# Kernel tuning notes

Measured on AMD Instinct MI355X. Metric: run time of the kernel, lower is better.

## Reference

```python
import jax, jax.numpy as jnp
import numpy as np

B, C, H, W = 8, 192, 64, 64
RED = 8
CR = C // RED  # 24


def prelu(x, a):
    # a is a single shared slope (PyTorch nn.PReLU() default num_parameters=1)
    return jnp.where(x >= 0, x, a * x)


def conv1x1(x, w, b):
    # x: [B,C,H,W], w: [O,C], b: [O] -> [B,O,H,W]
    return jnp.einsum('bchw,oc->bohw', x, w) + b[None, :, None, None]


def setup_inputs() -> dict:
    key = jax.random.key(0)
    ks = jax.random.split(key, 7)
    scale1 = 1.0 / np.sqrt(C)
    return {
        'x': jax.random.normal(ks[0], (B, C, H, W), dtype=jnp.float32),
        'w1': jax.random.uniform(ks[1], (CR, C), jnp.float32, -scale1, scale1),
        'b1': jnp.zeros((CR,), jnp.float32),
        'a1': jnp.full((1,), 0.25, jnp.float32),
        'w2': jax.random.uniform(ks[2], (CR, C), jnp.float32, -scale1, scale1),
        'b2': jnp.zeros((CR,), jnp.float32),
        'a2': jnp.full((1,), 0.25, jnp.float32),
        'wa': jax.random.uniform(ks[3], (C, C), jnp.float32, -scale1, scale1),
        'ba': jnp.zeros((C,), jnp.float32),
        'aa': jnp.full((1,), 0.25, jnp.float32),
    }


def reference(x, w1, b1, a1, w2, b2, a2, wa, ba, aa):
    b, c, h, w = x.shape
    hw = h * w
    q = prelu(conv1x1(x, w1, b1), a1)          # [B,Cr,H,W]
    k = prelu(conv1x1(x, w2, b2), a2)          # [B,Cr,H,W]
    v = prelu(conv1x1(x, wa, ba), aa)          # [B,C,H,W]
    q = q.reshape(b, -1, hw).transpose(0, 2, 1)   # [B,HW,Cr]
    k = k.reshape(b, -1, hw)                      # [B,Cr,HW]
    score = jax.nn.softmax(jnp.einsum('bnc,bcm->bnm', q, k), axis=2)  # [B,HW,HW]
    v = v.reshape(b, c, hw).transpose(0, 2, 1)    # [B,HW,C]
    out = jnp.einsum('bnm,bmc->bnc', score, v)    # [B,HW,C]
    return out.transpose(0, 2, 1).reshape(b, c, h, w)
```

## Files before the change

### kernel.cpp

```cpp
#include <hip/hip_runtime.h>
#include <hip/hip_fp16.h>

#define HW 4096
#define NC 192
#define NB 8
#define DQK 32
#define LOG2E 1.4426950408889634f
#define THR 8.0f

typedef _Float16 f16x8 __attribute__((ext_vector_type(8)));
typedef float f32x4 __attribute__((ext_vector_type(4)));
typedef unsigned int u32x4 __attribute__((ext_vector_type(4)));

static __device__ __forceinline__ unsigned int pkrtz(float a, float b) {
  auto h = __builtin_amdgcn_cvt_pkrtz(a, b);
  return __builtin_bit_cast(unsigned int, h);
}
static __device__ __forceinline__ unsigned short f2h_bits(float f) {
  _Float16 h = (_Float16)f;
  union { _Float16 h; unsigned short u; } cv; cv.h = h; return cv.u;
}

__global__ void wtrans_kernel(
    const float* __restrict__ w1, const float* __restrict__ b1, const float* __restrict__ a1,
    const float* __restrict__ w2, const float* __restrict__ b2, const float* __restrict__ a2,
    const float* __restrict__ wa, const float* __restrict__ ba, const float* __restrict__ aa,
    float* __restrict__ wt)
{
  const int c = blockIdx.x;
  const int o = threadIdx.x;
  if (o >= 240) return;
  float v;
  if (c < 192) {
    if (o < 24)      v = w1[o * 192 + c];
    else if (o < 48) v = w2[(o - 24) * 192 + c];
    else             v = wa[(o - 48) * 192 + c];
  } else if (c == 192) {
    v = (o < 24) ? b1[o] : (o < 48) ? b2[o - 24] : ba[o - 48];
  } else {
    v = (o < 24) ? a1[0] : (o < 48) ? a2[0] : aa[0];
  }
  wt[c * 240 + o] = v;
}

__global__ __launch_bounds__(256) void proj_kernel(
    const float* __restrict__ x, const float* __restrict__ wt,
    unsigned short* __restrict__ Qn, unsigned short* __restrict__ Kn,
    unsigned short* __restrict__ Vt)
{
  const int g   = blockIdx.y;
  const int tid = threadIdx.x;
  const int bp  = (blockIdx.x * 256 + tid) * 2;
  const int b   = bp >> 12;
  const int pos = bp & (HW - 1);

  const float* xb = x + (size_t)b * NC * HW + pos;
  float acc0[16], acc1[16];
  #pragma unroll
  for (int o = 0; o < 16; ++o) { acc0[o] = 0.f; acc1[o] = 0.f; }

  #pragma unroll 4
  for (int c = 0; c < 192; ++c) {
    float2 xv = *reinterpret_cast<const float2*>(xb + (size_t)c * HW);
    const float* wr = wt + c * 240 + g * 16;
    #pragma unroll
    for (int o = 0; o < 16; ++o) {
      float w = wr[o];
      acc0[o] = fmaf(w, xv.x, acc0[o]);
      acc1[o] = fmaf(w, xv.y, acc1[o]);
    }
  }

  const float* brow = wt + 192 * 240 + g * 16;
  const float* srow = wt + 193 * 240 + g * 16;
  unsigned short h0[16], h1[16];
  #pragma unroll
  for (int o = 0; o < 16; ++o) {
    float bias = brow[o], sm1 = srow[o] - 1.f;
    float v0 = acc0[o] + bias; v0 += fminf(v0, 0.f) * sm1;
    float v1 = acc1[o] + bias; v1 += fminf(v1, 0.f) * sm1;
    h0[o] = f2h_bits(v0);
    h1[o] = f2h_bits(v1);
  }

  if (g >= 3) {
    const int vch0 = g * 16 - 48;
    unsigned int* vp = reinterpret_cast<unsigned int*>(
        Vt + ((size_t)b * NC + vch0) * HW + pos);
    #pragma unroll
    for (int o = 0; o < 16; ++o)
      vp[o * (HW / 2)] = (unsigned int)h0[o] | ((unsigned int)h1[o] << 16);
  } else {
    u32x4 lo0, hi0, lo1, hi1;
    #pragma unroll
    for (int j = 0; j < 4; ++j) {
      lo0[j] = (unsigned int)h0[2 * j] | ((unsigned int)h0[2 * j + 1] << 16);
      hi0[j] = (unsigned int)h0[8 + 2 * j] | ((unsigned int)h0[9 + 2 * j] << 16);
      lo1[j] = (unsigned int)h1[2 * j] | ((unsigned int)h1[2 * j + 1] << 16);
      hi1[j] = (unsigned int)h1[8 + 2 * j] | ((unsigned int)h1[9 + 2 * j] << 16);
    }
    const size_t bpos = (size_t)b * HW + pos;
    if (g == 0) {
      u32x4* q0 = reinterpret_cast<u32x4*>(Qn + bpos * DQK);
      q0[0] = lo0; q0[1] = hi0;
      u32x4* q1 = reinterpret_cast<u32x4*>(Qn + (bpos + 1) * DQK);
      q1[0] = lo1; q1[1] = hi1;
    } else if (g == 1) {
      *reinterpret_cast<u32x4*>(Qn + bpos * DQK + 16) = lo0;
      *reinterpret_cast<u32x4*>(Kn + bpos * DQK) = hi0;
      *reinterpret_cast<u32x4*>(Qn + (bpos + 1) * DQK + 16) = lo1;
      *reinterpret_cast<u32x4*>(Kn + (bpos + 1) * DQK) = hi1;
    } else {
      u32x4* k0 = reinterpret_cast<u32x4*>(Kn + bpos * DQK + 8);
      k0[0] = lo0; k0[1] = hi0;
      u32x4* k1 = reinterpret_cast<u32x4*>(Kn + (bpos + 1) * DQK + 8);
      k1[0] = lo1; k1[1] = hi1;
    }
  }
}

__global__ __launch_bounds__(512, 4) void flash_kernel(
    const unsigned short* __restrict__ Qn, const unsigned short* __restrict__ Kn,
    const unsigned short* __restrict__ Vt, float* __restrict__ out)
{
  const int b    = blockIdx.y;
  const int q0   = blockIdx.x * 64;
  const int tid  = threadIdx.x;
  const int w    = tid >> 6;
  const int half = w >> 2;
  const int wi   = w & 3;
  const int lane = tid & 63;
  const int lq   = lane & 15;
  const int lk   = lane >> 4;

  __shared__ u32x4 Pex[2][4][2][64];
  __shared__ float alphaL[2][4][16];
  __shared__ float mlL[2][2][64];
  __shared__ f32x4 Obuf[4][64][13];

  const int mbase = half * (HW / 2);
  const int sigb  = 8 * (lq >> 2) + (lq & 3);

  f16x8 qfrag = *reinterpret_cast<const f16x8*>(
      Qn + ((size_t)b * HW + q0 + 16 * wi + lq) * DQK + 8 * lk);

  float m = -1e30f, l = 0.f;
  f32x4 O[12];
  #pragma unroll
  for (int i = 0; i < 12; ++i) O[i] = (f32x4){0.f, 0.f, 0.f, 0.f};

  const unsigned short* Kb = Kn + (size_t)b * HW * DQK;
  const unsigned short* Vb = Vt + (size_t)b * NC * HW;

  for (int it = 0; it < HW / 2 / 64; ++it) {
    const int m0 = mbase + it * 64;
    f32x4 s[4];
    #pragma unroll
    for (int t = 0; t < 4; ++t) {
      const int mo = m0 + sigb + 32 * (t & 1) + 4 * (t >> 1);
      f16x8 kf = *reinterpret_cast<const f16x8*>(Kb + (size_t)mo * DQK + 8 * lk);
      s[t] = __builtin_amdgcn_mfma_f32_16x16x32_f16(kf, qfrag,
              (f32x4){0.f, 0.f, 0.f, 0.f}, 0, 0, 0);
    }
    float pmax = s[0][0];
    #pragma unroll
    for (int t = 0; t < 4; ++t)
      #pragma unroll
      for (int r = 0; r < 4; ++r) pmax = fmaxf(pmax, s[t][r]);
    pmax = fmaxf(pmax, __shfl_xor(pmax, 16));
    pmax = fmaxf(pmax, __shfl_xor(pmax, 32));
    float alpha = 1.f;
    if (__any(pmax > m + THR)) {
      float mnew = fmaxf(m, pmax);
      alpha = __expf(m - mnew);
      m = mnew;
      l *= alpha;
    }
    if (lane < 16) alphaL[half][wi][lq] = alpha;
    const float mm = m * LOG2E;
    float psum = 0.f;
    f32x4 p[4];
    #pragma unroll
    for (int t = 0; t < 4; ++t)
      #pragma unroll
      for (int r = 0; r < 4; ++r) {
        p[t][r] = exp2f(fmaf(s[t][r], LOG2E, -mm));
        psum += p[t][r];
      }
    psum += __shfl_xor(psum, 16);
    psum += __shfl_xor(psum, 32);
    l += psum;
    u32x4 pa0, pa1;
    pa0[0] = pkrtz(p[0][0], p[0][1]); pa0[1] = pkrtz(p[0][2], p[0][3]);
    pa0[2] = pkrtz(p[2][0], p[2][1]); pa0[3] = pkrtz(p[2][2], p[2][3]);
    pa1[0] = pkrtz(p[1][0], p[1][1]); pa1[1] = pkrtz(p[1][2], p[1][3]);
    pa1[2] = pkrtz(p[3][0], p[3][1]); pa1[3] = pkrtz(p[3][2], p[3][3]);
    Pex[half][wi][0][lane] = pa0;
    Pex[half][wi][1][lane] = pa1;
    __syncthreads();
    #pragma unroll
    for (int tr = 0; tr < 4; ++tr) {
      f32x4 al = *reinterpret_cast<const f32x4*>(&alphaL[half][tr][4 * lk]);
      int diff = (al[0] != 1.f) | (al[1] != 1.f) | (al[2] != 1.f) | (al[3] != 1.f);
      if (__any(diff)) {
        #pragma unroll
        for (int tc = 0; tc < 3; ++tc) {
          O[tr * 3 + tc][0] *= al[0]; O[tr * 3 + tc][1] *= al[1];
          O[tr * 3 + tc][2] *= al[2]; O[tr * 3 + tc][3] *= al[3];
        }
      }
    }
    #pragma unroll
    for (int kk = 0; kk < 2; ++kk) {
      f16x8 paf[4];
      #pragma unroll
      for (int tr = 0; tr < 4; ++tr)
        paf[tr] = __builtin_bit_cast(f16x8, Pex[half][tr][kk][lane]);
      #pragma unroll
      for (int tc = 0; tc < 3; ++tc) {
        f16x8 vb = *reinterpret_cast<const f16x8*>(
            Vb + (size_t)(wi * 48 + tc * 16 + lq) * HW + m0 + kk * 32 + 8 * lk);
        #pragma unroll
        for (int tr = 0; tr < 4; ++tr)
          O[tr * 3 + tc] = __builtin_amdgcn_mfma_f32_16x16x32_f16(paf[tr], vb,
                               O[tr * 3 + tc], 0, 0, 0);
      }
    }
    __syncthreads();
  }

  if (lane < 16) {
    mlL[half][0][16 * wi + lq] = m;
    mlL[half][1][16 * wi + lq] = l;
  }
  if (half == 1) {
    #pragma unroll
    for (int i = 0; i < 12; ++i) Obuf[wi][lane][i] = O[i];
  }
  __syncthreads();
  if (half == 0) {
    #pragma unroll
    for (int tr = 0; tr < 4; ++tr) {
      f32x4 m0v = *reinterpret_cast<const f32x4*>(&mlL[0][0][16 * tr + 4 * lk]);
      f32x4 l0v = *reinterpret_cast<const f32x4*>(&mlL[0][1][16 * tr + 4 * lk]);
      f32x4 m1v = *reinterpret_cast<const f32x4*>(&mlL[1][0][16 * tr + 4 * lk]);
      f32x4 l1v = *reinterpret_cast<const f32x4*>(&mlL[1][1][16 * tr + 4 * lk]);
      f32x4 f0, f1;
      #pragma unroll
      for (int r = 0; r < 4; ++r) {
        float M  = fmaxf(m0v[r], m1v[r]);
        float s0 = __expf(m0v[r] - M), s1 = __expf(m1v[r] - M);
        float L  = s0 * l0v[r] + s1 * l1v[r];
        f0[r] = s0 / L; f1[r] = s1 / L;
      }
      #pragma unroll
      for (int tc = 0; tc < 3; ++tc) {
        f32x4 o1 = Obuf[wi][lane][tr * 3 + tc];
        f32x4 o;
        #pragma unroll
        for (int r = 0; r < 4; ++r)
          o[r] = O[tr * 3 + tc][r] * f0[r] + o1[r] * f1[r];
        *reinterpret_cast<f32x4*>(
            out + ((size_t)b * NC + wi * 48 + tc * 16 + lq) * HW + q0 + 16 * tr + 4 * lk) = o;
      }
    }
  }
}

extern "C" void kernel_launch(void* const* d_in, const int* in_sizes, int n_in,
                              void* d_out, int out_size, void* d_ws, size_t ws_size,
                              hipStream_t stream) {
  const float* x  = (const float*)d_in[0];
  const float* w1 = (const float*)d_in[1];
  const float* b1 = (const float*)d_in[2];
  const float* a1 = (const float*)d_in[3];
  const float* w2 = (const float*)d_in[4];
  const float* b2 = (const float*)d_in[5];
  const float* a2 = (const float*)d_in[6];
  const float* wa = (const float*)d_in[7];
  const float* ba = (const float*)d_in[8];
  const float* aa = (const float*)d_in[9];
  float* out = (float*)d_out;

  unsigned short* Qn = (unsigned short*)d_ws;
  unsigned short* Kn = Qn + (size_t)NB * HW * DQK;
  unsigned short* Vt = Kn + (size_t)NB * HW * DQK;
  float* wt = out + (out_size - 49152);

  (void)hipMemsetAsync(Qn, 0, (size_t)NB * HW * DQK * 2 * sizeof(unsigned short), stream);

  wtrans_kernel<<<dim3(194), 256, 0, stream>>>(w1, b1, a1, w2, b2, a2, wa, ba, aa, wt);

  dim3 pgrid(HW * NB / 512, 15);
  proj_kernel<<<pgrid, 256, 0, stream>>>(x, wt, Qn, Kn, Vt);

  dim3 fgrid(HW / 64, NB);
  flash_kernel<<<fgrid, 512, 0, stream>>>(Qn, Kn, Vt, out);
}
```

Measured before the change: 205.1 us.

## Software-pipeline flash loop with double-buffered P, register prefetch, MFMA row sums

Restructures the attention loop into a software pipeline. It prefetches the next K/V tiles into registers, computes the next block's QK and softmax while the current P·V runs, and double-buffers the P and alpha shared arrays so each iteration needs one barrier instead of two. The LOG2E scale is folded into Q during the projection kernel, and the row sum l is accumulated by an MFMA against a vector of ones instead of shuffles. The separate Obuf shared array is dropped and the final merge reuses the Pex storage in two passes, which lowers LDS use and may raise occupancy. In exchange, register pressure rises, and the row sum is now taken from the fp16-rounded P values.

```diff
diff --git a/kernel.cpp b/kernel.cpp
--- a/kernel.cpp
+++ b/kernel.cpp
@@ -6,11 +6,15 @@
 #define NB 8
 #define DQK 32
 #define LOG2E 1.4426950408889634f
-#define THR 8.0f
+#define THRL 11.541560327f
 
 typedef _Float16 f16x8 __attribute__((ext_vector_type(8)));
 typedef float f32x4 __attribute__((ext_vector_type(4)));
 typedef unsigned int u32x4 __attribute__((ext_vector_type(4)));
+
+#define BAR() do { asm volatile("s_waitcnt lgkmcnt(0)" ::: "memory"); \
+                   __builtin_amdgcn_s_barrier();                      \
+                   asm volatile("" ::: "memory"); } while (0)
 
 static __device__ __forceinline__ unsigned int pkrtz(float a, float b) {
   auto h = __builtin_amdgcn_cvt_pkrtz(a, b);
@@ -79,6 +83,7 @@
     float bias = brow[o], sm1 = srow[o] - 1.f;
     float v0 = acc0[o] + bias; v0 += fminf(v0, 0.f) * sm1;
     float v1 = acc1[o] + bias; v1 += fminf(v1, 0.f) * sm1;
+    if (g * 16 + o < 24) { v0 *= LOG2E; v1 *= LOG2E; }
     h0[o] = f2h_bits(v0);
     h1[o] = f2h_bits(v1);
   }
@@ -133,10 +138,9 @@
   const int lq   = lane & 15;
   const int lk   = lane >> 4;
 
-  __shared__ u32x4 Pex[2][4][2][64];
-  __shared__ float alphaL[2][4][16];
+  __shared__ u32x4 Pex[2][2][4][2][64];
+  __shared__ float alphaL[2][2][4][16];
   __shared__ float mlL[2][2][64];
-  __shared__ f32x4 Obuf[4][64][13];
 
   const int mbase = half * (HW / 2);
   const int sigb  = 8 * (lq >> 2) + (lq & 3);
@@ -144,24 +148,27 @@
   f16x8 qfrag = *reinterpret_cast<const f16x8*>(
       Qn + ((size_t)b * HW + q0 + 16 * wi + lq) * DQK + 8 * lk);
 
-  float m = -1e30f, l = 0.f;
-  f32x4 O[12];
+  float m = -1e30f;
+  f32x4 O[12], lacc;
   #pragma unroll
   for (int i = 0; i < 12; ++i) O[i] = (f32x4){0.f, 0.f, 0.f, 0.f};
-
-  const unsigned short* Kb = Kn + (size_t)b * HW * DQK;
-  const unsigned short* Vb = Vt + (size_t)b * NC * HW;
-
-  for (int it = 0; it < HW / 2 / 64; ++it) {
-    const int m0 = mbase + it * 64;
+  lacc = (f32x4){0.f, 0.f, 0.f, 0.f};
+
+  const unsigned short* Kb = Kn + (size_t)b * HW * DQK + (size_t)sigb * DQK + 8 * lk;
+  const unsigned short* Vw = Vt + (size_t)b * NC * HW + (size_t)(wi * 48 + lq) * HW + 8 * lk;
+
+  f16x8 vones;
+  #pragma unroll
+  for (int i = 0; i < 8; ++i) vones[i] = (_Float16)1.0f;
+
+  f16x8 Kf[4], Vf[6];
+
+  auto qk_softmax = [&](int par) {
     f32x4 s[4];
     #pragma unroll
-    for (int t = 0; t < 4; ++t) {
-      const int mo = m0 + sigb + 32 * (t & 1) + 4 * (t >> 1);
-      f16x8 kf = *reinterpret_cast<const f16x8*>(Kb + (size_t)mo * DQK + 8 * lk);
-      s[t] = __builtin_amdgcn_mfma_f32_16x16x32_f16(kf, qfrag,
+    for (int t = 0; t < 4; ++t)
+      s[t] = __builtin_amdgcn_mfma_f32_16x16x32_f16(Kf[t], qfrag,
               (f32x4){0.f, 0.f, 0.f, 0.f}, 0, 0, 0);
-    }
     float pmax = s[0][0];
     #pragma unroll
     for (int t = 0; t < 4; ++t)
@@ -170,37 +177,59 @@
     pmax = fmaxf(pmax, __shfl_xor(pmax, 16));
     pmax = fmaxf(pmax, __shfl_xor(pmax, 32));
     float alpha = 1.f;
-    if (__any(pmax > m + THR)) {
-      float mnew = fmaxf(m, pmax);
-      alpha = __expf(m - mnew);
-      m = mnew;
-      l *= alpha;
-    }
-    if (lane < 16) alphaL[half][wi][lq] = alpha;
-    const float mm = m * LOG2E;
-    float psum = 0.f;
-    f32x4 p[4];
+    if (__any(pmax > m + THRL)) {
+      float mn = fmaxf(m, pmax);
+      alpha = exp2f(m - mn);
+      m = mn;
+    }
+    float p[4][4];
     #pragma unroll
     for (int t = 0; t < 4; ++t)
       #pragma unroll
-      for (int r = 0; r < 4; ++r) {
-        p[t][r] = exp2f(fmaf(s[t][r], LOG2E, -mm));
-        psum += p[t][r];
-      }
-    psum += __shfl_xor(psum, 16);
-    psum += __shfl_xor(psum, 32);
-    l += psum;
+      for (int r = 0; r < 4; ++r) p[t][r] = exp2f(s[t][r] - m);
     u32x4 pa0, pa1;
     pa0[0] = pkrtz(p[0][0], p[0][1]); pa0[1] = pkrtz(p[0][2], p[0][3]);
     pa0[2] = pkrtz(p[2][0], p[2][1]); pa0[3] = pkrtz(p[2][2], p[2][3]);
     pa1[0] = pkrtz(p[1][0], p[1][1]); pa1[1] = pkrtz(p[1][2], p[1][3]);
     pa1[2] = pkrtz(p[3][0], p[3][1]); pa1[3] = pkrtz(p[3][2], p[3][3]);
-    Pex[half][wi][0][lane] = pa0;
-    Pex[half][wi][1][lane] = pa1;
-    __syncthreads();
+    Pex[par][half][wi][0][lane] = pa0;
+    Pex[par][half][wi][1][lane] = pa1;
+    if (lane < 16) alphaL[par][half][wi][lane] = alpha;
+  };
+
+  #pragma unroll
+  for (int t = 0; t < 4; ++t)
+    Kf[t] = *reinterpret_cast<const f16x8*>(
+        Kb + (size_t)(mbase + 32 * (t & 1) + 4 * (t >> 1)) * DQK);
+  qk_softmax(0);
+  #pragma unroll
+  for (int kk = 0; kk < 2; ++kk)
+    #pragma unroll
+    for (int tc = 0; tc < 3; ++tc)
+      Vf[kk * 3 + tc] = *reinterpret_cast<const f16x8*>(
+          Vw + (size_t)tc * 16 * HW + mbase + kk * 32);
+  BAR();
+
+  const int NIT = HW / 2 / 64;
+  for (int it = 0; it < NIT; ++it) {
+    const int p = it & 1;
+    const bool notlast = (it + 1 < NIT);
+    const int mnext = mbase + (it + 1) * 64;
+    if (notlast) {
+      #pragma unroll
+      for (int t = 0; t < 4; ++t)
+        Kf[t] = *reinterpret_cast<const f16x8*>(
+            Kb + (size_t)(mnext + 32 * (t & 1) + 4 * (t >> 1)) * DQK);
+    }
+    f16x8 paf[2][4];
+    #pragma unroll
+    for (int kk = 0; kk < 2; ++kk)
+      #pragma unroll
+      for (int tr = 0; tr < 4; ++tr)
+        paf[kk][tr] = __builtin_bit_cast(f16x8, Pex[p][half][tr][kk][lane]);
     #pragma unroll
     for (int tr = 0; tr < 4; ++tr) {
-      f32x4 al = *reinterpret_cast<const f32x4*>(&alphaL[half][tr][4 * lk]);
+      f32x4 al = *reinterpret_cast<const f32x4*>(&alphaL[p][half][tr][4 * lk]);
       int diff = (al[0] != 1.f) | (al[1] != 1.f) | (al[2] != 1.f) | (al[3] != 1.f);
       if (__any(diff)) {
         #pragma unroll
@@ -208,36 +237,46 @@
           O[tr * 3 + tc][0] *= al[0]; O[tr * 3 + tc][1] *= al[1];
           O[tr * 3 + tc][2] *= al[2]; O[tr * 3 + tc][3] *= al[3];
         }
+        if (tr == wi) {
+          lacc[0] *= al[0]; lacc[1] *= al[1]; lacc[2] *= al[2]; lacc[3] *= al[3];
+        }
       }
     }
     #pragma unroll
     for (int kk = 0; kk < 2; ++kk) {
-      f16x8 paf[4];
-      #pragma unroll
-      for (int tr = 0; tr < 4; ++tr)
-        paf[tr] = __builtin_bit_cast(f16x8, Pex[half][tr][kk][lane]);
-      #pragma unroll
-      for (int tc = 0; tc < 3; ++tc) {
-        f16x8 vb = *reinterpret_cast<const f16x8*>(
-            Vb + (size_t)(wi * 48 + tc * 16 + lq) * HW + m0 + kk * 32 + 8 * lk);
+      #pragma unroll
+      for (int tc = 0; tc < 3; ++tc)
         #pragma unroll
         for (int tr = 0; tr < 4; ++tr)
-          O[tr * 3 + tc] = __builtin_amdgcn_mfma_f32_16x16x32_f16(paf[tr], vb,
-                               O[tr * 3 + tc], 0, 0, 0);
-      }
-    }
-    __syncthreads();
-  }
-
-  if (lane < 16) {
-    mlL[half][0][16 * wi + lq] = m;
-    mlL[half][1][16 * wi + lq] = l;
-  }
+          O[tr * 3 + tc] = __builtin_amdgcn_mfma_f32_16x16x32_f16(
+              paf[kk][tr], Vf[kk * 3 + tc], O[tr * 3 + tc], 0, 0, 0);
+      f16x8 pw = __builtin_bit_cast(f16x8, Pex[p][half][wi][kk][lane]);
+      lacc = __builtin_amdgcn_mfma_f32_16x16x32_f16(pw, vones, lacc, 0, 0, 0);
+    }
+    if (notlast) {
+      #pragma unroll
+      for (int kk = 0; kk < 2; ++kk)
+        #pragma unroll
+        for (int tc = 0; tc < 3; ++tc)
+          Vf[kk * 3 + tc] = *reinterpret_cast<const f16x8*>(
+              Vw + (size_t)tc * 16 * HW + mnext + kk * 32);
+      qk_softmax(p ^ 1);
+    }
+    BAR();
+  }
+
+  if (lane < 16) mlL[half][0][16 * wi + lane] = m;
+  if (lq == 0) {
+    #pragma unroll
+    for (int r = 0; r < 4; ++r) mlL[half][1][16 * wi + 4 * lk + r] = lacc[r];
+  }
+  f32x4* Ost = reinterpret_cast<f32x4*>(&Pex[0][0][0][0][0]);
   if (half == 1) {
     #pragma unroll
-    for (int i = 0; i < 12; ++i) Obuf[wi][lane][i] = O[i];
-  }
-  __syncthreads();
+    for (int i = 0; i < 8; ++i) Ost[(wi * 8 + i) * 64 + lane] = O[i];
+  }
+  BAR();
+  f32x4 f0v[4], f1v[4];
   if (half == 0) {
     #pragma unroll
     for (int tr = 0; tr < 4; ++tr) {
@@ -245,24 +284,41 @@
       f32x4 l0v = *reinterpret_cast<const f32x4*>(&mlL[0][1][16 * tr + 4 * lk]);
       f32x4 m1v = *reinterpret_cast<const f32x4*>(&mlL[1][0][16 * tr + 4 * lk]);
       f32x4 l1v = *reinterpret_cast<const f32x4*>(&mlL[1][1][16 * tr + 4 * lk]);
-      f32x4 f0, f1;
       #pragma unroll
       for (int r = 0; r < 4; ++r) {
         float M  = fmaxf(m0v[r], m1v[r]);
-        float s0 = __expf(m0v[r] - M), s1 = __expf(m1v[r] - M);
+        float s0 = exp2f(m0v[r] - M), s1 = exp2f(m1v[r] - M);
         float L  = s0 * l0v[r] + s1 * l1v[r];
-        f0[r] = s0 / L; f1[r] = s1 / L;
+        f0v[tr][r] = s0 / L; f1v[tr][r] = s1 / L;
       }
-      #pragma unroll
-      for (int tc = 0; tc < 3; ++tc) {
-        f32x4 o1 = Obuf[wi][lane][tr * 3 + tc];
-        f32x4 o;
-        #pragma unroll
-        for (int r = 0; r < 4; ++r)
-          o[r] = O[tr * 3 + tc][r] * f0[r] + o1[r] * f1[r];
-        *reinterpret_cast<f32x4*>(
-            out + ((size_t)b * NC + wi * 48 + tc * 16 + lq) * HW + q0 + 16 * tr + 4 * lk) = o;
-      }
+    }
+    #pragma unroll
+    for (int i = 0; i < 8; ++i) {
+      const int tr = i / 3, tc = i - tr * 3;
+      f32x4 o1 = Ost[(wi * 8 + i) * 64 + lane];
+      f32x4 o;
+      #pragma unroll
+      for (int r = 0; r < 4; ++r) o[r] = O[i][r] * f0v[tr][r] + o1[r] * f1v[tr][r];
+      *reinterpret_cast<f32x4*>(
+          out + ((size_t)b * NC + wi * 48 + tc * 16 + lq) * HW + q0 + 16 * tr + 4 * lk) = o;
+    }
+  }
+  BAR();
+  if (half == 1) {
+    #pragma unroll
+    for (int i = 0; i < 4; ++i) Ost[(wi * 4 + i) * 64 + lane] = O[8 + i];
+  }
+  BAR();
+  if (half == 0) {
+    #pragma unroll
+    for (int i = 8; i < 12; ++i) {
+      const int tr = i / 3, tc = i - tr * 3;
+      f32x4 o1 = Ost[(wi * 4 + (i - 8)) * 64 + lane];
+      f32x4 o;
+      #pragma unroll
+      for (int r = 0; r < 4; ++r) o[r] = O[i][r] * f0v[tr][r] + o1[r] * f1v[tr][r];
+      *reinterpret_cast<f32x4*>(
+          out + ((size_t)b * NC + wi * 48 + tc * 16 + lq) * HW + q0 + 16 * tr + 4 * lk) = o;
     }
   }
 }
```

New measurement: 332.5 us. +62.1%, slower.
